# Optimization experiments

Measured on AMD Instinct MI355X. Metric: run time of the kernel, lower is better.

The kernel has to match this reference:

```python
import jax, jax.numpy as jnp
import numpy as np
from jax import lax

THRESHOLD_ABS = 0.5
MIN_DISTANCE = 3
MAX_PEAKS = 65536  # fixed-size peak buffer (jit-compatible replacement for torch nonzero)


def setup_inputs() -> dict:
    key = jax.random.key(0)
    belive_map = jax.random.uniform(key, (8, 2, 1024, 1024), dtype=jnp.float32)
    return {"belive_map": belive_map}


def reference(belive_map):
    B, C, H, W = belive_map.shape
    k = 2 * MIN_DISTANCE + 1  # 7
    pad = k // 2
    # max_pool2d(kernel=7, stride=1, padding=3) == sliding-window max with -inf padding
    x_max = lax.reduce_window(
        belive_map, -jnp.inf, lax.max,
        window_dimensions=(1, 1, k, k),
        window_strides=(1, 1, 1, 1),
        padding=((0, 0), (0, 0), (pad, pad), (pad, pad)),
    )
    x_mask = x_max == belive_map
    # exclude_border: zero a band of width 2*min_distance on all four sides
    ex = 2 * MIN_DISTANCE
    x_mask = x_mask.at[..., :ex].set(False)
    x_mask = x_mask.at[..., -ex:].set(False)
    x_mask = x_mask.at[..., :ex, :].set(False)
    x_mask = x_mask.at[..., -ex:, :].set(False)
    x_mask = x_mask & (belive_map > THRESHOLD_ABS)

    mask_flat = x_mask.reshape(B, C * H * W)
    val_flat = belive_map.reshape(B, C * H * W)

    def pick(m, v):
        # fixed-size nonzero; padded entries get index -1
        idx = jnp.nonzero(m, size=MAX_PEAKS, fill_value=-1)[0]
        valid = idx >= 0
        safe = jnp.where(valid, idx, 0)
        scores = jnp.where(valid, v[safe], 0.0)
        c = safe // (H * W)
        rem = safe % (H * W)
        h = rem // W
        w = rem % W
        coords = jnp.stack([w, h], axis=-1)           # (x, y) == ind[:, [2, 1]]
        coords = jnp.where(valid[:, None], coords, -1)
        labels = jnp.where(valid, c + 1, 0)            # ind[:, 0] + 1
        return coords, labels, scores

    coordinates, labels, scores = jax.vmap(pick)(mask_flat, val_flat)
    # per-image (coordinates, labels, scores), batched with fixed MAX_PEAKS slots;
    # invalid slots: coords=-1, labels=0, scores=0
    return coordinates, labels, scores
```

## Files before the change

### kernel.cpp

```cpp
#include <hip/hip_runtime.h>

#define HW  (1024u*1024u)
#define CHW (2u*HW)
#define MAXP 65536u
#define LABEL_OFF 1048576u
#define SCORE_OFF 1572864u
#define NINF (-3.0e38f)

__device__ __forceinline__ float max3f(float a, float b, float c) {
    return fmaxf(fmaxf(a, b), c);
}

__global__ __launch_bounds__(256, 4) void mask_kernel(const float* __restrict__ map,
                                                      unsigned* __restrict__ bits32,
                                                      unsigned* __restrict__ chunkCount) {
    __shared__ float4 rowbuf[2][2][258];
    __shared__ unsigned sred[4];
    int bid0 = blockIdx.x;
    int bid = (bid0 & 7) * 128 + (bid0 >> 3);
    int tid = threadIdx.x;
    int stripe = bid & 63;
    int img = bid >> 6;
    int r0 = stripe << 4;
    int lane = tid & 63, wv = tid >> 6;
    const float4* __restrict__ base = (const float4*)(map + ((size_t)img << 20));

    if (tid < 8) {
        float4 n4 = make_float4(NINF, NINF, NINF, NINF);
        rowbuf[(tid >> 2) & 1][(tid >> 1) & 1][(tid & 1) * 257] = n4;
    }

    int c0 = tid * 4;
    int cvm = 0;
    #pragma unroll
    for (int j = 0; j < 4; ++j) {
        int cc = c0 + j;
        if (cc >= 6 && cc <= 1017) cvm |= (1 << j);
    }

    float4 w[12];
    #pragma unroll
    for (int k = 0; k < 10; ++k) {
        int rr = r0 - 3 + k;
        w[k] = ((unsigned)rr < 1024u) ? base[rr * 256 + tid]
                                      : make_float4(NINF, NINF, NINF, NINF);
    }

    unsigned cnt = 0;

    #pragma unroll
    for (int p = 0; p < 8; ++p) {
        int rA = r0 + 2 * p;
        if (p < 6) {
            int q1 = rA + 7, q2 = rA + 8;
            w[(2 * p + 10) % 12] = ((unsigned)q1 < 1024u) ? base[q1 * 256 + tid]
                                                          : make_float4(NINF, NINF, NINF, NINF);
            w[(2 * p + 11) % 12] = ((unsigned)q2 < 1024u) ? base[q2 * 256 + tid]
                                                          : make_float4(NINF, NINF, NINF, NINF);
        }
        float4 s0 = w[(2 * p + 0) % 12], s1 = w[(2 * p + 1) % 12];
        float4 s2 = w[(2 * p + 2) % 12], s3 = w[(2 * p + 3) % 12];
        float4 s4 = w[(2 * p + 4) % 12], s5 = w[(2 * p + 5) % 12];
        float4 s6 = w[(2 * p + 6) % 12], s7 = w[(2 * p + 7) % 12];

        float4 c6, vmA, vmB;
        c6.x = fmaxf(max3f(s1.x, s2.x, s3.x), max3f(s4.x, s5.x, s6.x));
        c6.y = fmaxf(max3f(s1.y, s2.y, s3.y), max3f(s4.y, s5.y, s6.y));
        c6.z = fmaxf(max3f(s1.z, s2.z, s3.z), max3f(s4.z, s5.z, s6.z));
        c6.w = fmaxf(max3f(s1.w, s2.w, s3.w), max3f(s4.w, s5.w, s6.w));
        vmA.x = fmaxf(c6.x, s0.x); vmB.x = fmaxf(c6.x, s7.x);
        vmA.y = fmaxf(c6.y, s0.y); vmB.y = fmaxf(c6.y, s7.y);
        vmA.z = fmaxf(c6.z, s0.z); vmB.z = fmaxf(c6.z, s7.z);
        vmA.w = fmaxf(c6.w, s0.w); vmB.w = fmaxf(c6.w, s7.w);

        rowbuf[p & 1][0][tid + 1] = vmA;
        rowbuf[p & 1][1][tid + 1] = vmB;
        __syncthreads();
        float4 LA = rowbuf[p & 1][0][tid], RA = rowbuf[p & 1][0][tid + 2];
        float4 LB = rowbuf[p & 1][1][tid], RB = rowbuf[p & 1][1][tid + 2];

        float mA0 = max3f(max3f(LA.y, LA.z, LA.w),  max3f(vmA.x, vmA.y, vmA.z), vmA.w);
        float mA1 = max3f(max3f(LA.z, LA.w, vmA.x), max3f(vmA.y, vmA.z, vmA.w), RA.x);
        float mA2 = max3f(max3f(LA.w, vmA.x, vmA.y), max3f(vmA.z, vmA.w, RA.x), RA.y);
        float mA3 = max3f(max3f(vmA.x, vmA.y, vmA.z), max3f(vmA.w, RA.x, RA.y), RA.z);
        float mB0 = max3f(max3f(LB.y, LB.z, LB.w),  max3f(vmB.x, vmB.y, vmB.z), vmB.w);
        float mB1 = max3f(max3f(LB.z, LB.w, vmB.x), max3f(vmB.y, vmB.z, vmB.w), RB.x);
        float mB2 = max3f(max3f(LB.w, vmB.x, vmB.y), max3f(vmB.z, vmB.w, RB.x), RB.y);
        float mB3 = max3f(max3f(vmB.x, vmB.y, vmB.z), max3f(vmB.w, RB.x, RB.y), RB.z);

        float4 ctrA = s3, ctrB = s4;
        int fA0 = (ctrA.x == mA0) & (ctrA.x > 0.5f);
        int fA1 = (ctrA.y == mA1) & (ctrA.y > 0.5f);
        int fA2 = (ctrA.z == mA2) & (ctrA.z > 0.5f);
        int fA3 = (ctrA.w == mA3) & (ctrA.w > 0.5f);
        int fB0 = (ctrB.x == mB0) & (ctrB.x > 0.5f);
        int fB1 = (ctrB.y == mB1) & (ctrB.y > 0.5f);
        int fB2 = (ctrB.z == mB2) & (ctrB.z > 0.5f);
        int fB3 = (ctrB.w == mB3) & (ctrB.w > 0.5f);
        int nibA = (fA0 | (fA1 << 1) | (fA2 << 2) | (fA3 << 3)) & cvm;
        int nibB = (fB0 | (fB1 << 1) | (fB2 << 2) | (fB3 << 3)) & cvm;
        int rowokA = (rA >= 6) & (rA <= 1017);
        int rowokB = ((rA + 1) >= 6) & ((rA + 1) <= 1017);
        nibA = rowokA ? nibA : 0;
        nibB = rowokB ? nibB : 0;

        cnt += (unsigned)(__popc((unsigned)nibA) + __popc((unsigned)nibB));

        unsigned vA = (unsigned)nibA << ((lane & 7) * 4);
        unsigned vB = (unsigned)nibB << ((lane & 7) * 4);
        vA |= __shfl_xor(vA, 1, 64); vB |= __shfl_xor(vB, 1, 64);
        vA |= __shfl_xor(vA, 2, 64); vB |= __shfl_xor(vB, 2, 64);
        vA |= __shfl_xor(vA, 4, 64); vB |= __shfl_xor(vB, 4, 64);
        if ((lane & 7) == 0) {
            size_t wbase = ((size_t)img << 15) + ((size_t)rA << 5) + wv * 8 + (lane >> 3);
            bits32[wbase]      = vA;
            bits32[wbase + 32] = vB;
        }
    }

    for (int off = 32; off; off >>= 1) cnt += __shfl_down(cnt, off, 64);
    if (lane == 0) sred[wv] = cnt;
    __syncthreads();
    if (tid == 0) chunkCount[(img << 6) + stripe] = sred[0] + sred[1] + sred[2] + sred[3];
}

__global__ __launch_bounds__(256) void scan_scatter(const float* __restrict__ map,
                                                    const unsigned long long* __restrict__ bits,
                                                    const unsigned* __restrict__ chunkCount,
                                                    float* __restrict__ out) {
    int blk = blockIdx.x;
    int b = blk >> 7, cib = blk & 127;
    int tid = threadIdx.x;
    int lane = tid & 63, wv = tid >> 6;

    __shared__ unsigned long long sw[4];
    __shared__ unsigned sbase, stotal;
    __shared__ int wsum[4];

    unsigned cc = (tid < 128) ? chunkCount[b * 128 + tid] : 0u;
    unsigned long long v = ((tid < cib) ? (unsigned long long)cc : 0ull)
                         | ((unsigned long long)cc << 32);
    for (int off = 32; off; off >>= 1) v += __shfl_down(v, off, 64);
    if (lane == 0) sw[wv] = v;
    __syncthreads();
    if (tid == 0) {
        unsigned long long t = sw[0] + sw[1] + sw[2] + sw[3];
        sbase  = (unsigned)t;
        stotal = (unsigned)(t >> 32);
    }

    unsigned long long wd = bits[(size_t)blk * 256 + tid];
    int cnt = __popcll(wd);
    int incl = cnt;
    #pragma unroll
    for (int off = 1; off < 64; off <<= 1) {
        int n = __shfl_up(incl, off, 64);
        if (lane >= off) incl += n;
    }
    if (lane == 63) wsum[wv] = incl;
    __syncthreads();

    int wpre = 0;
    #pragma unroll
    for (int k = 0; k < 4; ++k) if (k < wv) wpre += wsum[k];
    unsigned base = sbase + (unsigned)wpre + (unsigned)(incl - cnt);
    unsigned wib = ((unsigned)cib) * 256u + (unsigned)tid;

    unsigned long long m = wd;
    unsigned n = 0;
    while (m) {
        int bit = __builtin_ctzll(m);
        m &= m - 1;
        unsigned slot = base + n;
        n++;
        if (slot < MAXP) {
            unsigned flat = wib * 64u + (unsigned)bit;
            unsigned c = flat >> 20;
            unsigned h = (flat >> 10) & 1023u;
            unsigned w = flat & 1023u;
            float score = map[(size_t)b * CHW + flat];
            unsigned o = b * MAXP + slot;
            out[2u * o]         = (float)w;
            out[2u * o + 1]     = (float)h;
            out[LABEL_OFF + o]  = (float)(c + 1u);
            out[SCORE_OFF + o]  = score;
        }
    }

    unsigned total = stotal;
    #pragma unroll
    for (int k = 0; k < 2; ++k) {
        unsigned slot = ((unsigned)cib) * 512u + (unsigned)tid + (unsigned)k * 256u;
        if (slot >= total) {
            unsigned o = b * MAXP + slot;
            float2 neg1; neg1.x = -1.0f; neg1.y = -1.0f;
            ((float2*)out)[o]   = neg1;
            out[LABEL_OFF + o]  = 0.0f;
            out[SCORE_OFF + o]  = 0.0f;
        }
    }
}

extern "C" void kernel_launch(void* const* d_in, const int* in_sizes, int n_in,
                              void* d_out, int out_size, void* d_ws, size_t ws_size,
                              hipStream_t stream) {
    const float* map = (const float*)d_in[0];
    float* out = (float*)d_out;
    unsigned long long* bits = (unsigned long long*)d_ws;
    unsigned* chunkCount = (unsigned*)((char*)d_ws + 2097152);

    mask_kernel<<<1024, 256, 0, stream>>>(map, (unsigned*)d_ws, chunkCount);
    scan_scatter<<<1024, 256, 0, stream>>>(map, bits, chunkCount, out);
}
```

Measured before the change: 33.10 us.

## Process four rows per barrier and prefetch deeper; swizzle scatter block order

The mask kernel now computes vertical maxima for four output rows per shared-memory phase instead of two, which halves the number of __syncthreads. Loads for the next four input rows are issued after the barrier, using an 18-entry register ring, so memory latency overlaps with the horizontal max work. The scatter kernel takes the same XCD-style block swizzle as the mask kernel, so bits written by one die are read back by blocks on that die, which should help L2 locality. The price is more registers and twice the LDS per block, which may lower occupancy under launch_bounds(256,4).

Measured after the change: 35.11 us. 6.1% more time.

```diff
diff --git a/kernel.cpp b/kernel.cpp
--- a/kernel.cpp
+++ b/kernel.cpp
@@ -14,7 +14,7 @@
 __global__ __launch_bounds__(256, 4) void mask_kernel(const float* __restrict__ map,
                                                       unsigned* __restrict__ bits32,
                                                       unsigned* __restrict__ chunkCount) {
-    __shared__ float4 rowbuf[2][2][258];
+    __shared__ float4 rowbuf[2][4][258];
     __shared__ unsigned sred[4];
     int bid0 = blockIdx.x;
     int bid = (bid0 & 7) * 128 + (bid0 >> 3);
@@ -24,10 +24,10 @@
     int r0 = stripe << 4;
     int lane = tid & 63, wv = tid >> 6;
     const float4* __restrict__ base = (const float4*)(map + ((size_t)img << 20));
-
-    if (tid < 8) {
-        float4 n4 = make_float4(NINF, NINF, NINF, NINF);
-        rowbuf[(tid >> 2) & 1][(tid >> 1) & 1][(tid & 1) * 257] = n4;
+    const float4 ninf4 = make_float4(NINF, NINF, NINF, NINF);
+
+    if (tid < 16) {
+        rowbuf[(tid >> 3) & 1][(tid >> 1) & 3][(tid & 1) * 257] = ninf4;
     }
 
     int c0 = tid * 4;
@@ -38,97 +38,110 @@
         if (cc >= 6 && cc <= 1017) cvm |= (1 << j);
     }
 
-    float4 w[12];
-    #pragma unroll
-    for (int k = 0; k < 10; ++k) {
+    float4 w[18];
+    #pragma unroll
+    for (int k = 0; k < 14; ++k) {
         int rr = r0 - 3 + k;
-        w[k] = ((unsigned)rr < 1024u) ? base[rr * 256 + tid]
-                                      : make_float4(NINF, NINF, NINF, NINF);
+        w[k] = ((unsigned)rr < 1024u) ? base[rr * 256 + tid] : ninf4;
     }
 
     unsigned cnt = 0;
 
     #pragma unroll
-    for (int p = 0; p < 8; ++p) {
-        int rA = r0 + 2 * p;
-        if (p < 6) {
-            int q1 = rA + 7, q2 = rA + 8;
-            w[(2 * p + 10) % 12] = ((unsigned)q1 < 1024u) ? base[q1 * 256 + tid]
-                                                          : make_float4(NINF, NINF, NINF, NINF);
-            w[(2 * p + 11) % 12] = ((unsigned)q2 < 1024u) ? base[q2 * 256 + tid]
-                                                          : make_float4(NINF, NINF, NINF, NINF);
-        }
-        float4 s0 = w[(2 * p + 0) % 12], s1 = w[(2 * p + 1) % 12];
-        float4 s2 = w[(2 * p + 2) % 12], s3 = w[(2 * p + 3) % 12];
-        float4 s4 = w[(2 * p + 4) % 12], s5 = w[(2 * p + 5) % 12];
-        float4 s6 = w[(2 * p + 6) % 12], s7 = w[(2 * p + 7) % 12];
-
-        float4 c6, vmA, vmB;
-        c6.x = fmaxf(max3f(s1.x, s2.x, s3.x), max3f(s4.x, s5.x, s6.x));
-        c6.y = fmaxf(max3f(s1.y, s2.y, s3.y), max3f(s4.y, s5.y, s6.y));
-        c6.z = fmaxf(max3f(s1.z, s2.z, s3.z), max3f(s4.z, s5.z, s6.z));
-        c6.w = fmaxf(max3f(s1.w, s2.w, s3.w), max3f(s4.w, s5.w, s6.w));
-        vmA.x = fmaxf(c6.x, s0.x); vmB.x = fmaxf(c6.x, s7.x);
-        vmA.y = fmaxf(c6.y, s0.y); vmB.y = fmaxf(c6.y, s7.y);
-        vmA.z = fmaxf(c6.z, s0.z); vmB.z = fmaxf(c6.z, s7.z);
-        vmA.w = fmaxf(c6.w, s0.w); vmB.w = fmaxf(c6.w, s7.w);
-
-        rowbuf[p & 1][0][tid + 1] = vmA;
-        rowbuf[p & 1][1][tid + 1] = vmB;
+    for (int s = 0; s < 4; ++s) {
+        #pragma unroll
+        for (int q = 0; q < 2; ++q) {
+            const int o = 4 * s + 2 * q;
+            float4 s0 = w[(o + 0) % 18], s1 = w[(o + 1) % 18];
+            float4 s2 = w[(o + 2) % 18], s3 = w[(o + 3) % 18];
+            float4 s4 = w[(o + 4) % 18], s5 = w[(o + 5) % 18];
+            float4 s6 = w[(o + 6) % 18], s7 = w[(o + 7) % 18];
+            float4 c6, vmA, vmB;
+            c6.x = fmaxf(max3f(s1.x, s2.x, s3.x), max3f(s4.x, s5.x, s6.x));
+            c6.y = fmaxf(max3f(s1.y, s2.y, s3.y), max3f(s4.y, s5.y, s6.y));
+            c6.z = fmaxf(max3f(s1.z, s2.z, s3.z), max3f(s4.z, s5.z, s6.z));
+            c6.w = fmaxf(max3f(s1.w, s2.w, s3.w), max3f(s4.w, s5.w, s6.w));
+            vmA.x = fmaxf(c6.x, s0.x); vmB.x = fmaxf(c6.x, s7.x);
+            vmA.y = fmaxf(c6.y, s0.y); vmB.y = fmaxf(c6.y, s7.y);
+            vmA.z = fmaxf(c6.z, s0.z); vmB.z = fmaxf(c6.z, s7.z);
+            vmA.w = fmaxf(c6.w, s0.w); vmB.w = fmaxf(c6.w, s7.w);
+            rowbuf[s & 1][2 * q][tid + 1]     = vmA;
+            rowbuf[s & 1][2 * q + 1][tid + 1] = vmB;
+        }
         __syncthreads();
-        float4 LA = rowbuf[p & 1][0][tid], RA = rowbuf[p & 1][0][tid + 2];
-        float4 LB = rowbuf[p & 1][1][tid], RB = rowbuf[p & 1][1][tid + 2];
-
-        float mA0 = max3f(max3f(LA.y, LA.z, LA.w),  max3f(vmA.x, vmA.y, vmA.z), vmA.w);
-        float mA1 = max3f(max3f(LA.z, LA.w, vmA.x), max3f(vmA.y, vmA.z, vmA.w), RA.x);
-        float mA2 = max3f(max3f(LA.w, vmA.x, vmA.y), max3f(vmA.z, vmA.w, RA.x), RA.y);
-        float mA3 = max3f(max3f(vmA.x, vmA.y, vmA.z), max3f(vmA.w, RA.x, RA.y), RA.z);
-        float mB0 = max3f(max3f(LB.y, LB.z, LB.w),  max3f(vmB.x, vmB.y, vmB.z), vmB.w);
-        float mB1 = max3f(max3f(LB.z, LB.w, vmB.x), max3f(vmB.y, vmB.z, vmB.w), RB.x);
-        float mB2 = max3f(max3f(LB.w, vmB.x, vmB.y), max3f(vmB.z, vmB.w, RB.x), RB.y);
-        float mB3 = max3f(max3f(vmB.x, vmB.y, vmB.z), max3f(vmB.w, RB.x, RB.y), RB.z);
-
-        float4 ctrA = s3, ctrB = s4;
-        int fA0 = (ctrA.x == mA0) & (ctrA.x > 0.5f);
-        int fA1 = (ctrA.y == mA1) & (ctrA.y > 0.5f);
-        int fA2 = (ctrA.z == mA2) & (ctrA.z > 0.5f);
-        int fA3 = (ctrA.w == mA3) & (ctrA.w > 0.5f);
-        int fB0 = (ctrB.x == mB0) & (ctrB.x > 0.5f);
-        int fB1 = (ctrB.y == mB1) & (ctrB.y > 0.5f);
-        int fB2 = (ctrB.z == mB2) & (ctrB.z > 0.5f);
-        int fB3 = (ctrB.w == mB3) & (ctrB.w > 0.5f);
-        int nibA = (fA0 | (fA1 << 1) | (fA2 << 2) | (fA3 << 3)) & cvm;
-        int nibB = (fB0 | (fB1 << 1) | (fB2 << 2) | (fB3 << 3)) & cvm;
-        int rowokA = (rA >= 6) & (rA <= 1017);
-        int rowokB = ((rA + 1) >= 6) & ((rA + 1) <= 1017);
-        nibA = rowokA ? nibA : 0;
-        nibB = rowokB ? nibB : 0;
-
-        cnt += (unsigned)(__popc((unsigned)nibA) + __popc((unsigned)nibB));
-
-        unsigned vA = (unsigned)nibA << ((lane & 7) * 4);
-        unsigned vB = (unsigned)nibB << ((lane & 7) * 4);
-        vA |= __shfl_xor(vA, 1, 64); vB |= __shfl_xor(vB, 1, 64);
-        vA |= __shfl_xor(vA, 2, 64); vB |= __shfl_xor(vB, 2, 64);
-        vA |= __shfl_xor(vA, 4, 64); vB |= __shfl_xor(vB, 4, 64);
-        if ((lane & 7) == 0) {
-            size_t wbase = ((size_t)img << 15) + ((size_t)rA << 5) + wv * 8 + (lane >> 3);
-            bits32[wbase]      = vA;
-            bits32[wbase + 32] = vB;
+
+        if (s < 2) {
+            #pragma unroll
+            for (int k = 0; k < 4; ++k) {
+                int rr = r0 + 11 + 4 * s + k;
+                w[(14 + 4 * s + k) % 18] = ((unsigned)rr < 1024u) ? base[rr * 256 + tid]
+                                                                  : ninf4;
+            }
+        }
+
+        #pragma unroll
+        for (int q = 0; q < 2; ++q) {
+            const int o = 4 * s + 2 * q;
+            int rA = r0 + o;
+            float4 VA = rowbuf[s & 1][2 * q][tid + 1];
+            float4 LA = rowbuf[s & 1][2 * q][tid];
+            float4 RA = rowbuf[s & 1][2 * q][tid + 2];
+            float4 VB = rowbuf[s & 1][2 * q + 1][tid + 1];
+            float4 LB = rowbuf[s & 1][2 * q + 1][tid];
+            float4 RB = rowbuf[s & 1][2 * q + 1][tid + 2];
+
+            float mA0 = max3f(max3f(LA.y, LA.z, LA.w),  max3f(VA.x, VA.y, VA.z), VA.w);
+            float mA1 = max3f(max3f(LA.z, LA.w, VA.x),  max3f(VA.y, VA.z, VA.w), RA.x);
+            float mA2 = max3f(max3f(LA.w, VA.x, VA.y),  max3f(VA.z, VA.w, RA.x), RA.y);
+            float mA3 = max3f(max3f(VA.x, VA.y, VA.z),  max3f(VA.w, RA.x, RA.y), RA.z);
+            float mB0 = max3f(max3f(LB.y, LB.z, LB.w),  max3f(VB.x, VB.y, VB.z), VB.w);
+            float mB1 = max3f(max3f(LB.z, LB.w, VB.x),  max3f(VB.y, VB.z, VB.w), RB.x);
+            float mB2 = max3f(max3f(LB.w, VB.x, VB.y),  max3f(VB.z, VB.w, RB.x), RB.y);
+            float mB3 = max3f(max3f(VB.x, VB.y, VB.z),  max3f(VB.w, RB.x, RB.y), RB.z);
+
+            float4 ctrA = w[(o + 3) % 18], ctrB = w[(o + 4) % 18];
+            int fA0 = (ctrA.x == mA0) & (ctrA.x > 0.5f);
+            int fA1 = (ctrA.y == mA1) & (ctrA.y > 0.5f);
+            int fA2 = (ctrA.z == mA2) & (ctrA.z > 0.5f);
+            int fA3 = (ctrA.w == mA3) & (ctrA.w > 0.5f);
+            int fB0 = (ctrB.x == mB0) & (ctrB.x > 0.5f);
+            int fB1 = (ctrB.y == mB1) & (ctrB.y > 0.5f);
+            int fB2 = (ctrB.z == mB2) & (ctrB.z > 0.5f);
+            int fB3 = (ctrB.w == mB3) & (ctrB.w > 0.5f);
+            int nibA = (fA0 | (fA1 << 1) | (fA2 << 2) | (fA3 << 3)) & cvm;
+            int nibB = (fB0 | (fB1 << 1) | (fB2 << 2) | (fB3 << 3)) & cvm;
+            int rowokA = (rA >= 6) & (rA <= 1017);
+            int rowokB = ((rA + 1) >= 6) & ((rA + 1) <= 1017);
+            nibA = rowokA ? nibA : 0;
+            nibB = rowokB ? nibB : 0;
+
+            cnt += (unsigned)(__popc((unsigned)nibA) + __popc((unsigned)nibB));
+
+            unsigned vA = (unsigned)nibA << ((lane & 7) * 4);
+            unsigned vB = (unsigned)nibB << ((lane & 7) * 4);
+            vA |= __shfl_xor(vA, 1, 64); vB |= __shfl_xor(vB, 1, 64);
+            vA |= __shfl_xor(vA, 2, 64); vB |= __shfl_xor(vB, 2, 64);
+            vA |= __shfl_xor(vA, 4, 64); vB |= __shfl_xor(vB, 4, 64);
+            if ((lane & 7) == 0) {
+                size_t wbase = ((size_t)img << 15) + ((size_t)rA << 5) + wv * 8 + (lane >> 3);
+                bits32[wbase]      = vA;
+                bits32[wbase + 32] = vB;
+            }
         }
     }
 
     for (int off = 32; off; off >>= 1) cnt += __shfl_down(cnt, off, 64);
     if (lane == 0) sred[wv] = cnt;
     __syncthreads();
-    if (tid == 0) chunkCount[(img << 6) + stripe] = sred[0] + sred[1] + sred[2] + sred[3];
+    if (tid == 0) chunkCount[bid] = sred[0] + sred[1] + sred[2] + sred[3];
 }
 
 __global__ __launch_bounds__(256) void scan_scatter(const float* __restrict__ map,
                                                     const unsigned long long* __restrict__ bits,
                                                     const unsigned* __restrict__ chunkCount,
                                                     float* __restrict__ out) {
-    int blk = blockIdx.x;
+    int bid0 = blockIdx.x;
+    int blk = (bid0 & 7) * 128 + (bid0 >> 3);
     int b = blk >> 7, cib = blk & 127;
     int tid = threadIdx.x;
     int lane = tid & 63, wv = tid >> 6;
@@ -177,10 +190,10 @@
             unsigned flat = wib * 64u + (unsigned)bit;
             unsigned c = flat >> 20;
             unsigned h = (flat >> 10) & 1023u;
-            unsigned w = flat & 1023u;
+            unsigned wcol = flat & 1023u;
             float score = map[(size_t)b * CHW + flat];
             unsigned o = b * MAXP + slot;
-            out[2u * o]         = (float)w;
+            out[2u * o]         = (float)wcol;
             out[2u * o + 1]     = (float)h;
             out[LABEL_OFF + o]  = (float)(c + 1u);
             out[SCORE_OFF + o]  = score;
```

## Fuse mask and scatter into one kernel with decoupled lookback prefix

Applied to the files above, without the earlier changes.

Merges the peak-mask kernel and the scan/scatter kernel into one. Each block keeps its bitmask tile in shared memory, publishes its count with a release-store, and spins on earlier blocks' counts to get its output base, which removes the global bitmask round-trip. A memset clears the counters, and a small trailing kernel writes the padding slots. The spin-wait relies on lower-indexed blocks being scheduled first, which risks deadlock or stalls if they are not resident, and it adds a memset launch.

New measurement: 85.53 us. 158% more time.

```diff
diff --git a/kernel.cpp b/kernel.cpp
--- a/kernel.cpp
+++ b/kernel.cpp
@@ -11,23 +11,28 @@
     return fmaxf(fmaxf(a, b), c);
 }
 
-__global__ __launch_bounds__(256, 4) void mask_kernel(const float* __restrict__ map,
-                                                      unsigned* __restrict__ bits32,
-                                                      unsigned* __restrict__ chunkCount) {
+__global__ __launch_bounds__(256, 4) void fused_nms(const float* __restrict__ map,
+                                                    unsigned* chunkCount,
+                                                    float* __restrict__ out) {
     __shared__ float4 rowbuf[2][2][258];
+    __shared__ __align__(8) unsigned lbits[512];
     __shared__ unsigned sred[4];
+    __shared__ unsigned swred[4];
+    __shared__ int wsum[4];
+
     int bid0 = blockIdx.x;
-    int bid = (bid0 & 7) * 128 + (bid0 >> 3);
+    int b = bid0 & 7;
+    int cib = bid0 >> 3;
+    int img = b * 2 + (cib >> 6);
+    int stripe = cib & 63;
+    int r0 = stripe << 4;
     int tid = threadIdx.x;
-    int stripe = bid & 63;
-    int img = bid >> 6;
-    int r0 = stripe << 4;
     int lane = tid & 63, wv = tid >> 6;
     const float4* __restrict__ base = (const float4*)(map + ((size_t)img << 20));
+    const float4 ninf4 = make_float4(NINF, NINF, NINF, NINF);
 
     if (tid < 8) {
-        float4 n4 = make_float4(NINF, NINF, NINF, NINF);
-        rowbuf[(tid >> 2) & 1][(tid >> 1) & 1][(tid & 1) * 257] = n4;
+        rowbuf[(tid >> 2) & 1][(tid >> 1) & 1][(tid & 1) * 257] = ninf4;
     }
 
     int c0 = tid * 4;
@@ -42,8 +47,7 @@
     #pragma unroll
     for (int k = 0; k < 10; ++k) {
         int rr = r0 - 3 + k;
-        w[k] = ((unsigned)rr < 1024u) ? base[rr * 256 + tid]
-                                      : make_float4(NINF, NINF, NINF, NINF);
+        w[k] = ((unsigned)rr < 1024u) ? base[rr * 256 + tid] : ninf4;
     }
 
     unsigned cnt = 0;
@@ -53,10 +57,8 @@
         int rA = r0 + 2 * p;
         if (p < 6) {
             int q1 = rA + 7, q2 = rA + 8;
-            w[(2 * p + 10) % 12] = ((unsigned)q1 < 1024u) ? base[q1 * 256 + tid]
-                                                          : make_float4(NINF, NINF, NINF, NINF);
-            w[(2 * p + 11) % 12] = ((unsigned)q2 < 1024u) ? base[q2 * 256 + tid]
-                                                          : make_float4(NINF, NINF, NINF, NINF);
+            w[(2 * p + 10) % 12] = ((unsigned)q1 < 1024u) ? base[q1 * 256 + tid] : ninf4;
+            w[(2 * p + 11) % 12] = ((unsigned)q2 < 1024u) ? base[q2 * 256 + tid] : ninf4;
         }
         float4 s0 = w[(2 * p + 0) % 12], s1 = w[(2 * p + 1) % 12];
         float4 s2 = w[(2 * p + 2) % 12], s3 = w[(2 * p + 3) % 12];
@@ -112,46 +114,38 @@
         vA |= __shfl_xor(vA, 2, 64); vB |= __shfl_xor(vB, 2, 64);
         vA |= __shfl_xor(vA, 4, 64); vB |= __shfl_xor(vB, 4, 64);
         if ((lane & 7) == 0) {
-            size_t wbase = ((size_t)img << 15) + ((size_t)rA << 5) + wv * 8 + (lane >> 3);
-            bits32[wbase]      = vA;
-            bits32[wbase + 32] = vB;
+            int widx = (2 * p) * 32 + wv * 8 + (lane >> 3);
+            lbits[widx]      = vA;
+            lbits[widx + 32] = vB;
         }
     }
 
     for (int off = 32; off; off >>= 1) cnt += __shfl_down(cnt, off, 64);
     if (lane == 0) sred[wv] = cnt;
     __syncthreads();
-    if (tid == 0) chunkCount[(img << 6) + stripe] = sred[0] + sred[1] + sred[2] + sred[3];
-}
-
-__global__ __launch_bounds__(256) void scan_scatter(const float* __restrict__ map,
-                                                    const unsigned long long* __restrict__ bits,
-                                                    const unsigned* __restrict__ chunkCount,
-                                                    float* __restrict__ out) {
-    int blk = blockIdx.x;
-    int b = blk >> 7, cib = blk & 127;
-    int tid = threadIdx.x;
-    int lane = tid & 63, wv = tid >> 6;
-
-    __shared__ unsigned long long sw[4];
-    __shared__ unsigned sbase, stotal;
-    __shared__ int wsum[4];
-
-    unsigned cc = (tid < 128) ? chunkCount[b * 128 + tid] : 0u;
-    unsigned long long v = ((tid < cib) ? (unsigned long long)cc : 0ull)
-                         | ((unsigned long long)cc << 32);
-    for (int off = 32; off; off >>= 1) v += __shfl_down(v, off, 64);
-    if (lane == 0) sw[wv] = v;
-    __syncthreads();
     if (tid == 0) {
-        unsigned long long t = sw[0] + sw[1] + sw[2] + sw[3];
-        sbase  = (unsigned)t;
-        stotal = (unsigned)(t >> 32);
-    }
-
-    unsigned long long wd = bits[(size_t)blk * 256 + tid];
-    int cnt = __popcll(wd);
-    int incl = cnt;
+        unsigned tot = sred[0] + sred[1] + sred[2] + sred[3];
+        __hip_atomic_store(&chunkCount[(b << 7) + cib], tot + 1u,
+                           __ATOMIC_RELEASE, __HIP_MEMORY_SCOPE_AGENT);
+    }
+
+    unsigned myv = 0;
+    if (tid < cib) {
+        unsigned v;
+        do {
+            v = __hip_atomic_load(&chunkCount[(b << 7) + tid],
+                                  __ATOMIC_ACQUIRE, __HIP_MEMORY_SCOPE_AGENT);
+        } while (v == 0u);
+        myv = v - 1u;
+    }
+    for (int off = 32; off; off >>= 1) myv += __shfl_down(myv, off, 64);
+    if (lane == 0) swred[wv] = myv;
+    __syncthreads();
+    unsigned sbase = swred[0] + swred[1] + swred[2] + swred[3];
+
+    unsigned long long wd = ((const unsigned long long*)lbits)[tid];
+    int cnt2 = __popcll(wd);
+    int incl = cnt2;
     #pragma unroll
     for (int off = 1; off < 64; off <<= 1) {
         int n = __shfl_up(incl, off, 64);
@@ -163,7 +157,7 @@
     int wpre = 0;
     #pragma unroll
     for (int k = 0; k < 4; ++k) if (k < wv) wpre += wsum[k];
-    unsigned base = sbase + (unsigned)wpre + (unsigned)(incl - cnt);
+    unsigned obase = sbase + (unsigned)wpre + (unsigned)(incl - cnt2);
     unsigned wib = ((unsigned)cib) * 256u + (unsigned)tid;
 
     unsigned long long m = wd;
@@ -171,23 +165,37 @@
     while (m) {
         int bit = __builtin_ctzll(m);
         m &= m - 1;
-        unsigned slot = base + n;
+        unsigned slot = obase + n;
         n++;
         if (slot < MAXP) {
             unsigned flat = wib * 64u + (unsigned)bit;
             unsigned c = flat >> 20;
             unsigned h = (flat >> 10) & 1023u;
-            unsigned w = flat & 1023u;
+            unsigned wcol = flat & 1023u;
             float score = map[(size_t)b * CHW + flat];
             unsigned o = b * MAXP + slot;
-            out[2u * o]         = (float)w;
+            out[2u * o]         = (float)wcol;
             out[2u * o + 1]     = (float)h;
             out[LABEL_OFF + o]  = (float)(c + 1u);
             out[SCORE_OFF + o]  = score;
         }
     }
-
-    unsigned total = stotal;
+}
+
+__global__ __launch_bounds__(256) void tail_pad(const unsigned* __restrict__ chunkCount,
+                                                float* __restrict__ out) {
+    int bid = blockIdx.x;
+    int b = bid >> 7, cib = bid & 127;
+    int tid = threadIdx.x;
+    int lane = tid & 63, wv = tid >> 6;
+    __shared__ unsigned swred[4];
+
+    unsigned v = (tid < 128) ? (chunkCount[(b << 7) + tid] - 1u) : 0u;
+    for (int off = 32; off; off >>= 1) v += __shfl_down(v, off, 64);
+    if (lane == 0) swred[wv] = v;
+    __syncthreads();
+    unsigned total = swred[0] + swred[1] + swred[2] + swred[3];
+
     #pragma unroll
     for (int k = 0; k < 2; ++k) {
         unsigned slot = ((unsigned)cib) * 512u + (unsigned)tid + (unsigned)k * 256u;
@@ -206,9 +214,9 @@
                               hipStream_t stream) {
     const float* map = (const float*)d_in[0];
     float* out = (float*)d_out;
-    unsigned long long* bits = (unsigned long long*)d_ws;
-    unsigned* chunkCount = (unsigned*)((char*)d_ws + 2097152);
-
-    mask_kernel<<<1024, 256, 0, stream>>>(map, (unsigned*)d_ws, chunkCount);
-    scan_scatter<<<1024, 256, 0, stream>>>(map, bits, chunkCount, out);
-}
+    unsigned* chunkCount = (unsigned*)d_ws;
+
+    hipMemsetAsync(d_ws, 0, 4096, stream);
+    fused_nms<<<1024, 256, 0, stream>>>(map, chunkCount, out);
+    tail_pad<<<1024, 256, 0, stream>>>(chunkCount, out);
+}
```
